# Performance work log

Measured on AMD Instinct MI355X. Metric: run time of the kernel, lower is better.

The kernel has to match this reference:

```python
import jax, jax.numpy as jnp
import numpy as np
from jax import lax

HS, WS = 8, 8  # pattern_size


def setup_inputs() -> dict:
    key = jax.random.key(0)
    k1, k2, k3 = jax.random.split(key, 3)
    B, C, T, H, W = 2, 64, 16, 112, 112
    Cout, K = 64, 3
    x = jax.random.normal(k1, (B, C, T, H, W), dtype=jnp.float32)
    # one independent Conv3d weight/bias per (h, w) phase in the 8x8 pattern
    weight = jax.random.normal(k2, (HS, WS, Cout, C, K, K, K), dtype=jnp.float32) * 0.05
    bias = jax.random.normal(k3, (HS, WS, Cout), dtype=jnp.float32) * 0.05
    return {"x": x, "weight": weight, "bias": bias}


def reference(x, weight, bias):
    hs, ws = HS, WS
    B, C, T, H, W = x.shape
    Cout = weight.shape[2]
    # torch F.pad(x, (hs-1, hs-1, ws-1, ws-1, 1, 1)): W padded by hs-1, H by ws-1, T by 1
    paded = jnp.pad(x, ((0, 0), (0, 0), (1, 1), (ws - 1, ws - 1), (hs - 1, hs - 1)))
    Ho, Wo = H // hs, W // ws  # conv output spatial size per phase: (H-3)//8 + 1 = H//8
    rows = []
    for h in range(hs):
        cols = []
        for w in range(ws):
            sl = paded[:, :, :, h:H + h, w:W + w]  # [B, C, T+2, H, W]
            y = lax.conv_general_dilated(
                sl, weight[h, w],
                window_strides=(1, hs, ws), padding='VALID',
                dimension_numbers=('NCDHW', 'OIDHW', 'NCDHW'))  # [B, Cout, T, Ho, Wo]
            cols.append(y + bias[h, w][None, :, None, None, None])
        rows.append(jnp.stack(cols, 0))
    res = jnp.stack(rows, 0)  # [hs, ws, B, Cout, T, Ho, Wo]
    # out[:, :, :, h + hs*i, w + ws*j] = res[h, w, :, :, :, i, j]
    out = jnp.transpose(res, (2, 3, 4, 5, 0, 6, 1))  # [B, Cout, T, Ho, hs, Wo, ws]
    return out.reshape(B, Cout, T, H, W)
```

## Files before the change

kernel.cpp:

```cpp
#include <hip/hip_runtime.h>
#include <hip/hip_bf16.h>
#include <stdint.h>

typedef __attribute__((ext_vector_type(8))) short short8;
typedef __attribute__((ext_vector_type(4))) float f32x4;

#define XPP_BYTES 66355200ull
#define WPP_BYTES 14155776ull

__device__ __forceinline__ void gl2lds16(const void* g, void* l) {
    __builtin_amdgcn_global_load_lds(
        (const __attribute__((address_space(1))) unsigned int*)g,
        (__attribute__((address_space(3))) unsigned int*)l, 16, 0, 0);
}

__global__ __launch_bounds__(512)
void xform_x(const float* __restrict__ xin, __hip_bfloat16* __restrict__ xpp) {
    extern __shared__ __hip_bfloat16 Xl[];
    const int bid = blockIdx.x;
    const int rho = bid % 14, d = (bid / 14) % 16, b = bid / 224;
    const int tid = threadIdx.x;
    for (int f = tid; f < 64 * 8 * 28; f += 512) {
        int ci = f / 224, rem = f % 224;
        int r = rem / 28, c4 = (rem % 28) * 4;
        const float4 v = *(const float4*)&xin[
            ((((size_t)b * 64 + ci) * 16 + d) * 112 + (rho * 8 + r)) * 112 + c4];
        const float vv[4] = {v.x, v.y, v.z, v.w};
#pragma unroll
        for (int u = 0; u < 4; ++u) {
            int c = c4 + u;
            Xl[(r * 112 + c) * 64 + (ci ^ ((c & 7) << 3))] = __float2bfloat16(vv[u]);
        }
    }
    __syncthreads();
    for (int f = tid; f < 896 * 8; f += 512) {
        int pos = f >> 3, j = f & 7;
        int r = pos / 112, c = pos % 112;
        int cw = c & 7, cwo = c >> 3;
        uint4 v = *(const uint4*)&Xl[pos * 64 + ((j * 8) ^ ((c & 7) << 3))];
        size_t dst = (((((size_t)(r * 8 + cw) * 2 + b) * 15 + (rho + 1)) * 15
                       + (cwo + 1)) * 18 + (d + 1)) * 64 + j * 8;
        *(uint4*)(xpp + dst) = v;
    }
}

__global__ __launch_bounds__(256)
void xform_w(const float* __restrict__ wt, __hip_bfloat16* __restrict__ wpp) {
    __shared__ __hip_bfloat16 lw[8 * 27 * 72];
    const int hw = blockIdx.x >> 3, cc = blockIdx.x & 7;
    for (int f = threadIdx.x; f < 8 * 64 * 27; f += 256) {
        int k = f % 27, ci = (f / 27) % 64, co = f / (27 * 64);
        float v = wt[(size_t)hw * 110592 + (size_t)(cc * 8 + co) * 1728 + ci * 27 + k];
        lw[(co * 27 + k) * 72 + ci] = __float2bfloat16(v);
    }
    __syncthreads();
    for (int f = threadIdx.x; f < 27 * 8 * 8; f += 256) {
        int cic = f % 8, co = (f / 8) % 8, k = f / 64;
        uint4 v = *(const uint4*)&lw[(co * 27 + k) * 72 + cic * 8];
        size_t dst = (((size_t)hw * 27 + k) * 64 + (cc * 8 + co)) * 64 + cic * 8;
        *(uint4*)(wpp + dst) = v;
    }
}

__global__ __launch_bounds__(256, 2)
void patgemm(const __hip_bfloat16* __restrict__ xpp,
             const __hip_bfloat16* __restrict__ wpp,
             const float* __restrict__ bs,
             float* __restrict__ out) {
    extern __shared__ char smem[];
    const int bid = blockIdx.x;
    const int h = bid & 7, k = bid >> 3;
    const int w = k & 7, b = (k >> 3) & 1, mc = k >> 4;
    const int hw = h * 8 + w;
    const int tid = threadIdx.x, wv = tid >> 6, lane = tid & 63;
    const int col = lane & 15, quad = lane >> 4;
    const int mg = wv >> 1, ng = wv & 1;

    uint32_t aoff[7], adst[7];
#pragma unroll
    for (int i = 0; i < 7; ++i) {
        int slot = tid + i * 256;
        int wo = slot >> 7, within = slot & 127;
        int rt = within >> 3, ch = within & 7;
        aoff[i] = (uint32_t)(wo * 2304 + rt * 128 + ((ch ^ (rt & 7)) << 4));
        adst[i] = (uint32_t)(slot * 16);
    }
    uint32_t boff[2], bdst[2];
#pragma unroll
    for (int i = 0; i < 2; ++i) {
        int slot = tid + i * 256;
        int co = slot >> 3, ch = slot & 7;
        boff[i] = (uint32_t)(co * 128 + ((ch ^ (co & 7)) << 4));
        bdst[i] = (uint32_t)(slot * 16);
    }
    uint32_t lofs[2];
#pragma unroll
    for (int ks = 0; ks < 2; ++ks)
        lofs[ks] = (uint32_t)(col * 128 + (((ks * 4 + quad) ^ (col & 7)) << 4));

    f32x4 acc[7][2];
#pragma unroll
    for (int j = 0; j < 7; ++j)
#pragma unroll
        for (int n = 0; n < 2; ++n) acc[j][n] = (f32x4){0.f, 0.f, 0.f, 0.f};

    const char* wbase = (const char*)wpp + (size_t)hw * 27 * 8192;

    auto STAGE = [&](int bi, int tap) {
        const int kd = tap / 9, kh = (tap / 3) % 3, kw = tap % 3;
        const int r0 = h + kh - 7, c0 = w + kw - 7;
        const int rh = r0 & 7, cw = c0 & 7;
        const int rho = (r0 >> 3) + 1 + mc, cwo = (c0 >> 3) + 1;
        const char* ap = (const char*)xpp +
            (size_t)((((rh * 8 + cw) * 2 + b) * 15 + rho) * 15 + cwo) * 2304
            + kd * 128;
        char* Ad = smem + bi * 28672;
#pragma unroll
        for (int i = 0; i < 7; ++i) gl2lds16(ap + aoff[i], Ad + adst[i]);
        const char* bp = wbase + (size_t)tap * 8192;
        char* Bd = smem + 57344 + bi * 8192;
#pragma unroll
        for (int i = 0; i < 2; ++i) gl2lds16(bp + boff[i], Bd + bdst[i]);
    };

    STAGE(0, 0);
    __syncthreads();

#pragma unroll 1
    for (int tap = 0; tap < 27; ++tap) {
        const int cur = tap & 1;
        if (tap < 26) STAGE(cur ^ 1, tap + 1);
        const char* Ab = smem + cur * 28672;
        const char* Bb = smem + 57344 + cur * 8192;
#pragma unroll
        for (int ks = 0; ks < 2; ++ks) {
            short8 bfr[2];
#pragma unroll
            for (int n = 0; n < 2; ++n)
                bfr[n] = *(const short8*)(Bb + (ng * 2 + n) * 2048 + lofs[ks]);
            short8 af[7];
#pragma unroll
            for (int j = 0; j < 7; ++j)
                af[j] = *(const short8*)(Ab + (mg * 7 + j) * 2048 + lofs[ks]);
            __builtin_amdgcn_s_setprio(1);
#pragma unroll
            for (int j = 0; j < 7; ++j)
#pragma unroll
                for (int n = 0; n < 2; ++n)
                    acc[j][n] = __builtin_amdgcn_mfma_f32_16x16x32_bf16(
                        af[j], bfr[n], acc[j][n], 0, 0, 0);
            __builtin_amdgcn_s_setprio(0);
        }
        __syncthreads();
    }

    const float* bsl = bs + hw * 64;
    const int y = 8 * mc + h;
#pragma unroll
    for (int j = 0; j < 7; ++j) {
        const int wo = mg * 7 + j;
        const int x = 8 * wo + w;
#pragma unroll
        for (int n = 0; n < 2; ++n) {
            const int co = (ng * 2 + n) * 16 + col;
            const float bv = bsl[co];
#pragma unroll
            for (int jj = 0; jj < 4; ++jj) {
                const int t = quad * 4 + jj;
                out[((((size_t)b * 64 + co) * 16 + t) * 112 + y) * 112 + x]
                    = acc[j][n][jj] + bv;
            }
        }
    }
}

#define XL_ROWSTRIDE 116
#define WL_WSTRIDE (17*27)

__global__ __launch_bounds__(256, 3)
void patconv3d_fp32(const float* __restrict__ xin,
                    const float* __restrict__ wt,
                    const float* __restrict__ bs,
                    float* __restrict__ out) {
    __shared__ float Xl[3*3*7*XL_ROWSTRIDE];
    __shared__ float Wl[8*WL_WSTRIDE];
    const int bid = blockIdx.x;
    const int ct = bid & 3, hb = (bid >> 2) & 1, h = (bid >> 3) & 7;
    const int t = (bid >> 6) & 15, b = (bid >> 10) & 1;
    const int tid = threadIdx.x;
    const int xl = tid & 127, cg = tid >> 7;
    const int xr = (xl < 112) ? xl : 111;
    const int wq = xl & 7;
    float acc[8][7];
#pragma unroll
    for (int c = 0; c < 8; ++c)
#pragma unroll
        for (int ho = 0; ho < 7; ++ho) acc[c][ho] = 0.f;
    for (int ci = 0; ci < 64; ++ci) {
        __syncthreads();
        for (int idx = tid; idx < 3 * 3 * 7 * 114; idx += 256) {
            int c = idx % 114, rest = idx / 114;
            int ho = rest % 7; rest /= 7;
            int kh = rest % 3, kd = rest / 3;
            int r = 8 * (hb * 7 + ho) + h + kh - 7;
            int d = t + kd - 1, colx = c - 7;
            float v = 0.f;
            if (r >= 0 && d >= 0 && d < 16 && colx >= 0)
                v = xin[(((size_t)(b * 64 + ci) * 16 + d) * 112 + r) * 112 + colx];
            Xl[((kd * 3 + kh) * 7 + ho) * XL_ROWSTRIDE + c] = v;
        }
        for (int idx = tid; idx < 8 * 16 * 27; idx += 256) {
            int k = idx % 27, rest = idx / 27;
            int co_l = rest % 16, wi = rest / 16;
            Wl[wi * WL_WSTRIDE + co_l * 27 + k] =
                wt[(((size_t)(h * 8 + wi) * 64 + (ct * 16 + co_l)) * 64 + ci) * 27 + k];
        }
        __syncthreads();
#pragma unroll
        for (int kd = 0; kd < 3; ++kd)
#pragma unroll
            for (int kh = 0; kh < 3; ++kh)
#pragma unroll
                for (int kw = 0; kw < 3; ++kw) {
                    const int k = (kd * 3 + kh) * 3 + kw;
                    float xv[7];
#pragma unroll
                    for (int ho = 0; ho < 7; ++ho)
                        xv[ho] = Xl[((kd * 3 + kh) * 7 + ho) * XL_ROWSTRIDE + xr + kw];
                    float wv[8];
#pragma unroll
                    for (int c = 0; c < 8; ++c)
                        wv[c] = Wl[wq * WL_WSTRIDE + (cg * 8 + c) * 27 + k];
#pragma unroll
                    for (int c = 0; c < 8; ++c)
#pragma unroll
                        for (int ho = 0; ho < 7; ++ho)
                            acc[c][ho] += wv[c] * xv[ho];
                }
    }
    if (xl < 112) {
#pragma unroll
        for (int c = 0; c < 8; ++c) {
            const int co = ct * 16 + cg * 8 + c;
            const float bv = bs[(h * 8 + wq) * 64 + co];
#pragma unroll
            for (int ho = 0; ho < 7; ++ho) {
                const int y = 8 * (hb * 7 + ho) + h;
                out[(((size_t)(b * 64 + co) * 16 + t) * 112 + y) * 112 + xl] = acc[c][ho] + bv;
            }
        }
    }
}

extern "C" void kernel_launch(void* const* d_in, const int* in_sizes, int n_in,
                              void* d_out, int out_size, void* d_ws, size_t ws_size,
                              hipStream_t stream) {
    const float* x  = (const float*)d_in[0];
    const float* wg = (const float*)d_in[1];
    const float* bi = (const float*)d_in[2];
    float* out = (float*)d_out;
    if (ws_size >= XPP_BYTES + WPP_BYTES) {
        __hip_bfloat16* xpp = (__hip_bfloat16*)d_ws;
        __hip_bfloat16* wpp = (__hip_bfloat16*)((char*)d_ws + XPP_BYTES);
        hipMemsetAsync(d_ws, 0, XPP_BYTES, stream);
        xform_x<<<448, 512, 114688, stream>>>(x, xpp);
        xform_w<<<512, 256, 0, stream>>>(wg, wpp);
        patgemm<<<1792, 256, 73728, stream>>>(xpp, wpp, bi, out);
    } else {
        patconv3d_fp32<<<2048, 256, 0, stream>>>(x, wg, bi, out);
    }
}
```

Baseline: 281.7 us.

## Stage A tile once per spatial tap and reuse across temporal taps

The GEMM loop now runs over 9 spatial (kh,kw) taps instead of 27. Each step stages an 18-row temporal window of the input tile into LDS, and the three temporal offsets kd are read from shifted rows of it. Weights are no longer staged through LDS; they are read straight from global memory into registers. The full workspace memset is replaced by a kernel that zeros only the padding regions. The aim is fewer LDS stage and barrier rounds, less redundant input traffic and a cheaper zero-fill, at the cost of more vector registers for weights and global-load latency on B.

```diff
diff --git a/kernel.cpp b/kernel.cpp
--- a/kernel.cpp
+++ b/kernel.cpp
@@ -6,12 +6,40 @@
 typedef __attribute__((ext_vector_type(4))) float f32x4;
 
 #define XPP_BYTES 66355200ull
+#define XPP_SLACK 65536ull
 #define WPP_BYTES 14155776ull
 
 __device__ __forceinline__ void gl2lds16(const void* g, void* l) {
     __builtin_amdgcn_global_load_lds(
         (const __attribute__((address_space(1))) unsigned int*)g,
         (__attribute__((address_space(3))) unsigned int*)l, 16, 0, 0);
+}
+
+__global__ __launch_bounds__(256)
+void bzero(uint4* __restrict__ xpp) {
+    const uint4 z = {0u, 0u, 0u, 0u};
+    const int total = 935936;
+    for (int idx = blockIdx.x * 256 + threadIdx.x; idx < total;
+         idx += gridDim.x * 256) {
+        int u;
+        if (idx < 276480) {
+            int slab = idx / 2160, off = idx % 2160;
+            u = slab * 32400 + off;
+        } else if (idx < 534528) {
+            int k = idx - 276480;
+            int run = k / 144, off = k % 144;
+            int slab = run / 14, rho = run % 14 + 1;
+            u = slab * 32400 + rho * 2160 + off;
+        } else {
+            int k = idx - 534528;
+            int run = k / 8, off = k % 8;
+            int slab = run / 392, r2 = run % 392;
+            int rho = r2 / 28 + 1, r3 = r2 % 28;
+            int cwo = r3 / 2 + 1, d = (r3 & 1) * 17;
+            u = slab * 32400 + rho * 2160 + cwo * 144 + d * 8 + off;
+        }
+        xpp[u] = z;
+    }
 }
 
 __global__ __launch_bounds__(512)
@@ -76,27 +104,22 @@
     const int col = lane & 15, quad = lane >> 4;
     const int mg = wv >> 1, ng = wv & 1;
 
-    uint32_t aoff[7], adst[7];
-#pragma unroll
-    for (int i = 0; i < 7; ++i) {
+    uint32_t aoff[8];
+#pragma unroll
+    for (int i = 0; i < 8; ++i) {
         int slot = tid + i * 256;
-        int wo = slot >> 7, within = slot & 127;
-        int rt = within >> 3, ch = within & 7;
+        int wo = slot / 144, rem = slot % 144;
+        int rt = rem >> 3, ch = rem & 7;
         aoff[i] = (uint32_t)(wo * 2304 + rt * 128 + ((ch ^ (rt & 7)) << 4));
-        adst[i] = (uint32_t)(slot * 16);
-    }
-    uint32_t boff[2], bdst[2];
-#pragma unroll
-    for (int i = 0; i < 2; ++i) {
-        int slot = tid + i * 256;
-        int co = slot >> 3, ch = slot & 7;
-        boff[i] = (uint32_t)(co * 128 + ((ch ^ (co & 7)) << 4));
-        bdst[i] = (uint32_t)(slot * 16);
-    }
-    uint32_t lofs[2];
-#pragma unroll
-    for (int ks = 0; ks < 2; ++ks)
-        lofs[ks] = (uint32_t)(col * 128 + (((ks * 4 + quad) ^ (col & 7)) << 4));
+    }
+    uint32_t rofs[3][2];
+#pragma unroll
+    for (int kd = 0; kd < 3; ++kd)
+#pragma unroll
+        for (int ks = 0; ks < 2; ++ks)
+            rofs[kd][ks] = (uint32_t)((col + kd) * 128
+                + (((ks * 4 + quad) ^ ((col + kd) & 7)) << 4));
+    const uint32_t bofs = (uint32_t)(col * 128 + quad * 16);
 
     f32x4 acc[7][2];
 #pragma unroll
@@ -106,50 +129,54 @@
 
     const char* wbase = (const char*)wpp + (size_t)hw * 27 * 8192;
 
-    auto STAGE = [&](int bi, int tap) {
-        const int kd = tap / 9, kh = (tap / 3) % 3, kw = tap % 3;
+    auto STAGE = [&](int bi, int rr) {
+        const int kh = rr / 3, kw = rr % 3;
         const int r0 = h + kh - 7, c0 = w + kw - 7;
-        const int rh = r0 & 7, cw = c0 & 7;
-        const int rho = (r0 >> 3) + 1 + mc, cwo = (c0 >> 3) + 1;
         const char* ap = (const char*)xpp +
-            (size_t)((((rh * 8 + cw) * 2 + b) * 15 + rho) * 15 + cwo) * 2304
-            + kd * 128;
-        char* Ad = smem + bi * 28672;
-#pragma unroll
-        for (int i = 0; i < 7; ++i) gl2lds16(ap + aoff[i], Ad + adst[i]);
-        const char* bp = wbase + (size_t)tap * 8192;
-        char* Bd = smem + 57344 + bi * 8192;
-#pragma unroll
-        for (int i = 0; i < 2; ++i) gl2lds16(bp + boff[i], Bd + bdst[i]);
+            (size_t)(((((r0 & 7) * 8 + (c0 & 7)) * 2 + b) * 15
+                      + ((r0 >> 3) + 1 + mc)) * 15 + ((c0 >> 3) + 1)) * 2304;
+        char* Ad = smem + bi * 32768;
+#pragma unroll
+        for (int i = 0; i < 8; ++i)
+            gl2lds16(ap + aoff[i], Ad + (uint32_t)(tid + i * 256) * 16);
     };
 
     STAGE(0, 0);
     __syncthreads();
 
 #pragma unroll 1
-    for (int tap = 0; tap < 27; ++tap) {
-        const int cur = tap & 1;
-        if (tap < 26) STAGE(cur ^ 1, tap + 1);
-        const char* Ab = smem + cur * 28672;
-        const char* Bb = smem + 57344 + cur * 8192;
-#pragma unroll
-        for (int ks = 0; ks < 2; ++ks) {
-            short8 bfr[2];
-#pragma unroll
-            for (int n = 0; n < 2; ++n)
-                bfr[n] = *(const short8*)(Bb + (ng * 2 + n) * 2048 + lofs[ks]);
-            short8 af[7];
-#pragma unroll
-            for (int j = 0; j < 7; ++j)
-                af[j] = *(const short8*)(Ab + (mg * 7 + j) * 2048 + lofs[ks]);
-            __builtin_amdgcn_s_setprio(1);
-#pragma unroll
-            for (int j = 0; j < 7; ++j)
+    for (int rr = 0; rr < 9; ++rr) {
+        const int cur = rr & 1;
+        short8 bfr[12];
+        const char* bp = wbase + (size_t)rr * 8192;
+#pragma unroll
+        for (int kd = 0; kd < 3; ++kd)
+#pragma unroll
+            for (int ks = 0; ks < 2; ++ks)
 #pragma unroll
                 for (int n = 0; n < 2; ++n)
-                    acc[j][n] = __builtin_amdgcn_mfma_f32_16x16x32_bf16(
-                        af[j], bfr[n], acc[j][n], 0, 0, 0);
-            __builtin_amdgcn_s_setprio(0);
+                    bfr[kd * 4 + ks * 2 + n] = *(const short8*)(
+                        bp + kd * 73728 + (ng * 2 + n) * 2048 + ks * 64 + bofs);
+        __builtin_amdgcn_sched_barrier(0);
+        if (rr < 8) STAGE(cur ^ 1, rr + 1);
+        const char* Ab = smem + cur * 32768;
+#pragma unroll
+        for (int kd = 0; kd < 3; ++kd) {
+#pragma unroll
+            for (int ks = 0; ks < 2; ++ks) {
+                short8 af[7];
+#pragma unroll
+                for (int j = 0; j < 7; ++j)
+                    af[j] = *(const short8*)(Ab + (mg * 7 + j) * 2304 + rofs[kd][ks]);
+                __builtin_amdgcn_s_setprio(1);
+#pragma unroll
+                for (int j = 0; j < 7; ++j)
+#pragma unroll
+                    for (int n = 0; n < 2; ++n)
+                        acc[j][n] = __builtin_amdgcn_mfma_f32_16x16x32_bf16(
+                            af[j], bfr[kd * 4 + ks * 2 + n], acc[j][n], 0, 0, 0);
+                __builtin_amdgcn_s_setprio(0);
+            }
         }
         __syncthreads();
     }
@@ -259,13 +286,13 @@
     const float* wg = (const float*)d_in[1];
     const float* bi = (const float*)d_in[2];
     float* out = (float*)d_out;
-    if (ws_size >= XPP_BYTES + WPP_BYTES) {
+    if (ws_size >= XPP_BYTES + XPP_SLACK + WPP_BYTES) {
         __hip_bfloat16* xpp = (__hip_bfloat16*)d_ws;
-        __hip_bfloat16* wpp = (__hip_bfloat16*)((char*)d_ws + XPP_BYTES);
-        hipMemsetAsync(d_ws, 0, XPP_BYTES, stream);
+        __hip_bfloat16* wpp = (__hip_bfloat16*)((char*)d_ws + XPP_BYTES + XPP_SLACK);
+        bzero<<<1024, 256, 0, stream>>>((uint4*)d_ws);
         xform_x<<<448, 512, 114688, stream>>>(x, xpp);
         xform_w<<<512, 256, 0, stream>>>(wg, wpp);
-        patgemm<<<1792, 256, 73728, stream>>>(xpp, wpp, bi, out);
+        patgemm<<<1792, 256, 65536, stream>>>(xpp, wpp, bi, out);
     } else {
         patconv3d_fp32<<<2048, 256, 0, stream>>>(x, wg, bi, out);
     }
```

Measured after the change: 294.9 us. 1.05x slower.
